# Optimization experiments

Hardware: AMD Instinct MI355X
Metric: run time of the kernel (lower is better)

## Reference

```python
import jax, jax.numpy as jnp
import numpy as np

B, C, T = 8, 64, 2048


def setup_inputs() -> dict:
    key = jax.random.key(0)
    eeg_data = jax.random.normal(key, (B, C, T), dtype=jnp.float32)
    return {"eeg_data": eeg_data}


def _hilbert(signal):
    # FFT-based analytic signal, faithful to the torch code:
    # zero frequencies >= n//2 (even n) or >= (n+1)//2 (odd n), then multiply ALL by 2.
    n = signal.shape[-1]
    spec = jnp.fft.fft(signal, axis=-1)
    cut = n // 2 if n % 2 == 0 else (n + 1) // 2
    keep = (jnp.arange(n) < cut).astype(spec.dtype)
    spec = spec * keep * 2
    return jnp.fft.ifft(spec, axis=-1)


def reference(eeg_data):
    b, c, t = eeg_data.shape
    analytic = _hilbert(eeg_data)
    phase = jnp.angle(analytic)                      # [B, C, T]
    # pairwise phase differences: [B, C, C, T]
    phase_diff = phase[:, :, None, :] - phase[:, None, :, :]
    sin_pd = jnp.sin(phase_diff)
    numerator = jnp.abs(jnp.mean(sin_pd, axis=-1))   # [B, C, C]
    denominator = jnp.mean(jnp.abs(sin_pd), axis=-1)
    denominator = jnp.where(denominator == 0, jnp.float32(1e-8), denominator)
    wpli = numerator / denominator
    eye_mask = 1.0 - jnp.eye(c, dtype=wpli.dtype)[None, :, :]
    return wpli * eye_mask
```

## Files before the change

kernel.cpp:

```cpp
#include <hip/hip_runtime.h>
#include <math.h>

#define T_LEN 2048
#define C_CH  64
#define B_N   8
#define NCHUNK 64

__device__ __forceinline__ float2 cadd(float2 a, float2 b) { return make_float2(a.x + b.x, a.y + b.y); }
__device__ __forceinline__ float2 csub(float2 a, float2 b) { return make_float2(a.x - b.x, a.y - b.y); }

template <int SIGN>
__device__ __forceinline__ void fft_stages(float2*& src, float2*& dst, int tid,
                                           const float2* tw1, const float2* tw2,
                                           const float2* tw3) {
  for (int n = T_LEN, ls = 0; n >= 4; n >>= 2, ls += 2) {
    const int s = 1 << ls;
    const int m = n >> 2;
    const int base = (T_LEN - n) / 3;
    for (int idx = tid; idx < T_LEN / 4; idx += 256) {
      const int p = idx >> ls;
      const int q = idx & (s - 1);
      const int ib = q + s * p;
      const float2 a = src[ib];
      const float2 b = src[ib + s * m];
      const float2 c = src[ib + 2 * s * m];
      const float2 d = src[ib + 3 * s * m];
      const float2 t0 = cadd(a, c);
      const float2 t1 = csub(a, c);
      const float2 t2 = cadd(b, d);
      const float2 t3 = csub(b, d);
      const float2 y0 = cadd(t0, t2);
      const float2 r2 = csub(t0, t2);
      float2 r1, r3;
      if (SIGN < 0) {
        r1 = make_float2(t1.x + t3.y, t1.y - t3.x);
        r3 = make_float2(t1.x - t3.y, t1.y + t3.x);
      } else {
        r1 = make_float2(t1.x - t3.y, t1.y + t3.x);
        r3 = make_float2(t1.x + t3.y, t1.y - t3.x);
      }
      const float2 w1 = tw1[base + p];
      const float2 w2 = tw2[base + p];
      const float2 w3 = tw3[base + p];
      const float c1 = w1.x, s1 = (SIGN < 0) ? w1.y : -w1.y;
      const float c2 = w2.x, s2 = (SIGN < 0) ? w2.y : -w2.y;
      const float c3 = w3.x, s3 = (SIGN < 0) ? w3.y : -w3.y;
      const float2 y1 = make_float2(r1.x * c1 - r1.y * s1, r1.x * s1 + r1.y * c1);
      const float2 y2 = make_float2(r2.x * c2 - r2.y * s2, r2.x * s2 + r2.y * c2);
      const float2 y3 = make_float2(r3.x * c3 - r3.y * s3, r3.x * s3 + r3.y * c3);
      const int ob = q + s * 4 * p;
      dst[ob]         = y0;
      dst[ob + s]     = y1;
      dst[ob + 2 * s] = y2;
      dst[ob + 3 * s] = y3;
    }
    __syncthreads();
    float2* tmp = src; src = dst; dst = tmp;
  }
  for (int q = tid; q < T_LEN / 2; q += 256) {
    const float2 a = src[q];
    const float2 b = src[q + T_LEN / 2];
    dst[q]             = cadd(a, b);
    dst[q + T_LEN / 2] = csub(a, b);
  }
  __syncthreads();
  float2* tmp = src; src = dst; dst = tmp;
}

__global__ __launch_bounds__(256) void hilbert_phasor_kernel(
    const float* __restrict__ x, float2* __restrict__ phasor) {
  __shared__ float2 bufA[T_LEN];
  __shared__ float2 bufB[T_LEN];
  __shared__ float2 tw1[682], tw2[682], tw3[682];

  const int bc = blockIdx.x;
  const int tid = threadIdx.x;
  const float* sig = x + (size_t)bc * T_LEN;

  for (int idx = tid; idx < 682; idx += 256) {
    int n, p;
    if (idx < 512)      { n = 2048; p = idx; }
    else if (idx < 640) { n = 512;  p = idx - 512; }
    else if (idx < 672) { n = 128;  p = idx - 640; }
    else if (idx < 680) { n = 32;   p = idx - 672; }
    else                { n = 8;    p = idx - 680; }
    const float th = -6.28318530717958647692f * (float)p / (float)n;
    float sn, cs;
    sincosf(th, &sn, &cs);        tw1[idx] = make_float2(cs, sn);
    sincosf(2.0f * th, &sn, &cs); tw2[idx] = make_float2(cs, sn);
    sincosf(3.0f * th, &sn, &cs); tw3[idx] = make_float2(cs, sn);
  }

  for (int t = tid; t < T_LEN; t += 256)
    bufA[t] = make_float2(sig[t], 0.0f);
  __syncthreads();

  float2* src = bufA;
  float2* dst = bufB;

  fft_stages<-1>(src, dst, tid, tw1, tw2, tw3);

  for (int k = tid; k < T_LEN; k += 256) {
    const float f = (k < T_LEN / 2) ? 2.0f : 0.0f;
    src[k].x *= f;
    src[k].y *= f;
  }
  __syncthreads();

  fft_stages<1>(src, dst, tid, tw1, tw2, tw3);

  for (int t = tid; t < T_LEN; t += 256) {
    const float2 z = src[t];
    const float mag2 = z.x * z.x + z.y * z.y;
    float u, v;
    if (mag2 > 0.0f) {
      const float inv = rsqrtf(mag2);
      u = z.x * inv;
      v = z.y * inv;
    } else {
      u = 1.0f;
      v = 0.0f;
    }
    phasor[(size_t)bc * T_LEN + t] = make_float2(u, v);
  }
}

__global__ __launch_bounds__(256) void wpli_partial_kernel(
    const float2* __restrict__ phasor, float2* __restrict__ part, int nchunk) {
  __shared__ float2 lz[32][65];

  const int c = blockIdx.x;
  const int b = blockIdx.y;
  const int tid = threadIdx.x;
  const int tx = tid & 15;
  const int ty = tid >> 4;

  float accn[4][4] = {{0}}, accd[4][4] = {{0}};

  for (int sub = c; sub < T_LEN / 32; sub += nchunk) {
    const int t0 = sub * 32;
    __syncthreads();
    for (int idx = tid; idx < 2048; idx += 256) {
      const int ch = idx >> 5;
      const int tt = idx & 31;
      lz[tt][ch] = phasor[((size_t)(b * C_CH + ch)) * T_LEN + t0 + tt];
    }
    __syncthreads();

    for (int tt = 0; tt < 32; ++tt) {
      float2 zi[4], zj[4];
#pragma unroll
      for (int a = 0; a < 4; ++a) {
        zi[a] = lz[tt][ty * 4 + a];
        zj[a] = lz[tt][tx * 4 + a];
      }
#pragma unroll
      for (int a = 0; a < 4; ++a)
#pragma unroll
        for (int e = 0; e < 4; ++e) {
          const float s = zi[a].y * zj[e].x - zi[a].x * zj[e].y;
          accn[a][e] += s;
          accd[a][e] += fabsf(s);
        }
    }
  }

  float2* dstp = part + ((size_t)c * B_N + b) * (C_CH * C_CH);
#pragma unroll
  for (int a = 0; a < 4; ++a)
#pragma unroll
    for (int e = 0; e < 4; ++e) {
      const int i = ty * 4 + a;
      const int j = tx * 4 + e;
      dstp[i * C_CH + j] = make_float2(accn[a][e], accd[a][e]);
    }
}

__global__ __launch_bounds__(256) void wpli_finalize_kernel(
    const float2* __restrict__ part, float* __restrict__ out, int nchunk) {
  const int idx = blockIdx.x * 256 + threadIdx.x;
  if (idx >= B_N * C_CH * C_CH) return;
  const int b = idx >> 12;
  const int pair = idx & 4095;
  float n = 0.0f, d = 0.0f;
  for (int c = 0; c < nchunk; ++c) {
    const float2 p = part[((size_t)c * B_N + b) * (C_CH * C_CH) + pair];
    n += p.x;
    d += p.y;
  }
  const int i = pair >> 6;
  const int j = pair & 63;
  float w = (d > 0.0f) ? fabsf(n) / d : 0.0f;
  if (i == j) w = 0.0f;
  out[idx] = w;
}

extern "C" void kernel_launch(void* const* d_in, const int* in_sizes, int n_in,
                              void* d_out, int out_size, void* d_ws, size_t ws_size,
                              hipStream_t stream) {
  const float* eeg = (const float*)d_in[0];
  float* out = (float*)d_out;

  const size_t phasor_bytes = (size_t)B_N * C_CH * T_LEN * sizeof(float2);
  float2* phasor = (float2*)d_ws;
  float2* part = (float2*)((char*)d_ws + phasor_bytes);

  const size_t per_chunk = (size_t)B_N * C_CH * C_CH * sizeof(float2);
  const size_t avail = (ws_size > phasor_bytes) ? ws_size - phasor_bytes : 0;
  int nchunk = NCHUNK;
  while (nchunk > 1 && (size_t)nchunk * per_chunk > avail) nchunk >>= 1;

  hilbert_phasor_kernel<<<B_N * C_CH, 256, 0, stream>>>(eeg, phasor);

  dim3 grid(nchunk, B_N);
  wpli_partial_kernel<<<grid, 256, 0, stream>>>(phasor, part, nchunk);

  wpli_finalize_kernel<<<(B_N * C_CH * C_CH + 255) / 256, 256, 0, stream>>>(
      part, out, nchunk);
}
```

Before: 102.4 us.

## Specialize Hilbert FFT: real-input first stage, pruned inverse, fused phasor output

Restructures the Hilbert FFT kernel. The first radix-4 stage reads the real signal directly, and the half-spectrum zeroing is folded into a reduced first inverse stage that only reads the nonzero half. The final radix-2 inverse stage is fused with phasor normalization and the store. Twiddle tables shrink to one, with w2 and w3 computed in registers, and padded shared-memory indexing is added to reduce bank conflicts. It trades extra FLOPs and indexing arithmetic for fewer shared-memory passes, barriers and less LDS usage.

```diff
diff --git a/kernel.cpp b/kernel.cpp
--- a/kernel.cpp
+++ b/kernel.cpp
@@ -6,25 +6,27 @@
 #define B_N   8
 #define NCHUNK 64
 
+#define IX(a) ((a) + ((a) >> 4))
+
 __device__ __forceinline__ float2 cadd(float2 a, float2 b) { return make_float2(a.x + b.x, a.y + b.y); }
 __device__ __forceinline__ float2 csub(float2 a, float2 b) { return make_float2(a.x - b.x, a.y - b.y); }
+__device__ __forceinline__ float2 cmul(float2 a, float2 w) {
+  return make_float2(a.x * w.x - a.y * w.y, a.x * w.y + a.y * w.x);
+}
 
 template <int SIGN>
-__device__ __forceinline__ void fft_stages(float2*& src, float2*& dst, int tid,
-                                           const float2* tw1, const float2* tw2,
-                                           const float2* tw3) {
-  for (int n = T_LEN, ls = 0; n >= 4; n >>= 2, ls += 2) {
+__device__ __forceinline__ void radix4_stages(float2*& src, float2*& dst,
+                                              int tid, const float2* tw) {
+  for (int n = 512, ls = 2; n >= 8; n >>= 2, ls += 2) {
     const int s = 1 << ls;
-    const int m = n >> 2;
     const int base = (T_LEN - n) / 3;
-    for (int idx = tid; idx < T_LEN / 4; idx += 256) {
+    for (int idx = tid; idx < 512; idx += 256) {
       const int p = idx >> ls;
       const int q = idx & (s - 1);
-      const int ib = q + s * p;
-      const float2 a = src[ib];
-      const float2 b = src[ib + s * m];
-      const float2 c = src[ib + 2 * s * m];
-      const float2 d = src[ib + 3 * s * m];
+      const float2 a = src[IX(idx)];
+      const float2 b = src[IX(idx + 512)];
+      const float2 c = src[IX(idx + 1024)];
+      const float2 d = src[IX(idx + 1536)];
       const float2 t0 = cadd(a, c);
       const float2 t1 = csub(a, c);
       const float2 t2 = cadd(b, d);
@@ -39,39 +41,26 @@
         r1 = make_float2(t1.x - t3.y, t1.y + t3.x);
         r3 = make_float2(t1.x + t3.y, t1.y - t3.x);
       }
-      const float2 w1 = tw1[base + p];
-      const float2 w2 = tw2[base + p];
-      const float2 w3 = tw3[base + p];
-      const float c1 = w1.x, s1 = (SIGN < 0) ? w1.y : -w1.y;
-      const float c2 = w2.x, s2 = (SIGN < 0) ? w2.y : -w2.y;
-      const float c3 = w3.x, s3 = (SIGN < 0) ? w3.y : -w3.y;
-      const float2 y1 = make_float2(r1.x * c1 - r1.y * s1, r1.x * s1 + r1.y * c1);
-      const float2 y2 = make_float2(r2.x * c2 - r2.y * s2, r2.x * s2 + r2.y * c2);
-      const float2 y3 = make_float2(r3.x * c3 - r3.y * s3, r3.x * s3 + r3.y * c3);
-      const int ob = q + s * 4 * p;
-      dst[ob]         = y0;
-      dst[ob + s]     = y1;
-      dst[ob + 2 * s] = y2;
-      dst[ob + 3 * s] = y3;
+      float2 w1 = tw[base + p];
+      if (SIGN > 0) w1.y = -w1.y;
+      const float2 w2 = make_float2(w1.x * w1.x - w1.y * w1.y, 2.0f * w1.x * w1.y);
+      const float2 w3 = cmul(w2, w1);
+      const int ob = q + 4 * s * p;
+      dst[IX(ob)]         = y0;
+      dst[IX(ob + s)]     = cmul(r1, w1);
+      dst[IX(ob + 2 * s)] = cmul(r2, w2);
+      dst[IX(ob + 3 * s)] = cmul(r3, w3);
     }
     __syncthreads();
     float2* tmp = src; src = dst; dst = tmp;
   }
-  for (int q = tid; q < T_LEN / 2; q += 256) {
-    const float2 a = src[q];
-    const float2 b = src[q + T_LEN / 2];
-    dst[q]             = cadd(a, b);
-    dst[q + T_LEN / 2] = csub(a, b);
-  }
-  __syncthreads();
-  float2* tmp = src; src = dst; dst = tmp;
 }
 
 __global__ __launch_bounds__(256) void hilbert_phasor_kernel(
     const float* __restrict__ x, float2* __restrict__ phasor) {
-  __shared__ float2 bufA[T_LEN];
-  __shared__ float2 bufB[T_LEN];
-  __shared__ float2 tw1[682], tw2[682], tw3[682];
+  __shared__ float2 bufA[IX(T_LEN - 1) + 1];
+  __shared__ float2 bufB[IX(T_LEN - 1) + 1];
+  __shared__ float2 tw[682];
 
   const int bc = blockIdx.x;
   const int tid = threadIdx.x;
@@ -84,44 +73,85 @@
     else if (idx < 672) { n = 128;  p = idx - 640; }
     else if (idx < 680) { n = 32;   p = idx - 672; }
     else                { n = 8;    p = idx - 680; }
-    const float th = -6.28318530717958647692f * (float)p / (float)n;
     float sn, cs;
-    sincosf(th, &sn, &cs);        tw1[idx] = make_float2(cs, sn);
-    sincosf(2.0f * th, &sn, &cs); tw2[idx] = make_float2(cs, sn);
-    sincosf(3.0f * th, &sn, &cs); tw3[idx] = make_float2(cs, sn);
-  }
-
-  for (int t = tid; t < T_LEN; t += 256)
-    bufA[t] = make_float2(sig[t], 0.0f);
-  __syncthreads();
+    sincosf(-6.28318530717958647692f * (float)p / (float)n, &sn, &cs);
+    tw[idx] = make_float2(cs, sn);
+  }
 
   float2* src = bufA;
   float2* dst = bufB;
 
-  fft_stages<-1>(src, dst, tid, tw1, tw2, tw3);
-
-  for (int k = tid; k < T_LEN; k += 256) {
-    const float f = (k < T_LEN / 2) ? 2.0f : 0.0f;
-    src[k].x *= f;
-    src[k].y *= f;
+  for (int idx = tid; idx < 512; idx += 256) {
+    const float a = sig[idx];
+    const float b = sig[idx + 512];
+    const float c = sig[idx + 1024];
+    const float d = sig[idx + 1536];
+    const float t0 = a + c, t1 = a - c, t2 = b + d, t3 = b - d;
+    const float2 w1 = tw[idx];
+    const float2 w2 = make_float2(w1.x * w1.x - w1.y * w1.y, 2.0f * w1.x * w1.y);
+    const float2 w3 = cmul(w2, w1);
+    const float2 r1 = make_float2(t1, -t3);
+    const float2 r3 = make_float2(t1,  t3);
+    src[IX(4 * idx)]     = make_float2(t0 + t2, 0.0f);
+    src[IX(4 * idx + 1)] = cmul(r1, w1);
+    src[IX(4 * idx + 2)] = make_float2((t0 - t2) * w2.x, (t0 - t2) * w2.y);
+    src[IX(4 * idx + 3)] = cmul(r3, w3);
   }
   __syncthreads();
 
-  fft_stages<1>(src, dst, tid, tw1, tw2, tw3);
-
-  for (int t = tid; t < T_LEN; t += 256) {
-    const float2 z = src[t];
-    const float mag2 = z.x * z.x + z.y * z.y;
-    float u, v;
-    if (mag2 > 0.0f) {
-      const float inv = rsqrtf(mag2);
-      u = z.x * inv;
-      v = z.y * inv;
-    } else {
-      u = 1.0f;
-      v = 0.0f;
-    }
-    phasor[(size_t)bc * T_LEN + t] = make_float2(u, v);
+  radix4_stages<-1>(src, dst, tid, tw);
+
+  for (int q = tid; q < 1024; q += 256) {
+    const float2 a = src[IX(q)];
+    const float2 b = src[IX(q + 1024)];
+    dst[IX(q)]        = cadd(a, b);
+    dst[IX(q + 1024)] = csub(a, b);
+  }
+  __syncthreads();
+  { float2* tmp = src; src = dst; dst = tmp; }
+
+  for (int idx = tid; idx < 512; idx += 256) {
+    const float2 a = src[IX(idx)];
+    const float2 b = src[IX(idx + 512)];
+    float2 w1 = tw[idx]; w1.y = -w1.y;
+    const float2 w2 = make_float2(w1.x * w1.x - w1.y * w1.y, 2.0f * w1.x * w1.y);
+    const float2 w3 = cmul(w2, w1);
+    const float2 y0 = cadd(a, b);
+    const float2 r2 = csub(a, b);
+    const float2 r1 = make_float2(a.x - b.y, a.y + b.x);
+    const float2 r3 = make_float2(a.x + b.y, a.y - b.x);
+    dst[IX(4 * idx)]     = y0;
+    dst[IX(4 * idx + 1)] = cmul(r1, w1);
+    dst[IX(4 * idx + 2)] = cmul(r2, w2);
+    dst[IX(4 * idx + 3)] = cmul(r3, w3);
+  }
+  __syncthreads();
+  { float2* tmp = src; src = dst; dst = tmp; }
+
+  radix4_stages<1>(src, dst, tid, tw);
+
+  for (int q = tid; q < 1024; q += 256) {
+    const float2 a = src[IX(q)];
+    const float2 b = src[IX(q + 1024)];
+    const float2 zs = cadd(a, b);
+    const float2 zd = csub(a, b);
+    float2 outv[2] = {zs, zd};
+    int    outq[2] = {q, q + 1024};
+#pragma unroll
+    for (int k = 0; k < 2; ++k) {
+      const float2 z = outv[k];
+      const float mag2 = z.x * z.x + z.y * z.y;
+      float u, v;
+      if (mag2 > 0.0f) {
+        const float inv = rsqrtf(mag2);
+        u = z.x * inv;
+        v = z.y * inv;
+      } else {
+        u = 1.0f;
+        v = 0.0f;
+      }
+      phasor[(size_t)bc * T_LEN + outq[k]] = make_float2(u, v);
+    }
   }
 }
 
```

New measurement: 99.85 us. 2.5% less time.
